# Performance work log

Hardware: AMD Instinct MI355X
Metric: run time of the kernel (lower is better)

Reference implementation:

```python
import jax, jax.numpy as jnp
import numpy as np


def _ln(x, g, b):
    m = x.mean(-1, keepdims=True)
    v = x.var(-1, keepdims=True)
    return (x - m) * jax.lax.rsqrt(v + 1e-5) * g + b


def _shift(x):
    # RWKV time-shift: xx[t] = x[t-1], xx[0] = 0
    return jnp.pad(x, ((0, 0), (1, 0), (0, 0)))[:, :-1]


def setup_inputs() -> dict:
    key = jax.random.key(0)
    ks = jax.random.split(key, 20)
    B, S, D, E, F = 2, 2048, 1024, 8, 2048
    s = 0.02
    return dict(
        x=jax.random.normal(ks[0], (B, S, D), jnp.float32),
        ln1_g=jnp.ones((D,), jnp.float32), ln1_b=jnp.zeros((D,), jnp.float32),
        ln2_g=jnp.ones((D,), jnp.float32), ln2_b=jnp.zeros((D,), jnp.float32),
        tm_mu_k=jax.random.uniform(ks[1], (D,), jnp.float32),
        tm_mu_v=jax.random.uniform(ks[2], (D,), jnp.float32),
        tm_mu_r=jax.random.uniform(ks[3], (D,), jnp.float32),
        time_decay=jax.random.normal(ks[4], (D,), jnp.float32) * 0.1,
        time_first=jax.random.normal(ks[5], (D,), jnp.float32) * 0.1,
        Wk=jax.random.normal(ks[6], (D, D), jnp.float32) * s,
        Wv=jax.random.normal(ks[7], (D, D), jnp.float32) * s,
        Wr=jax.random.normal(ks[8], (D, D), jnp.float32) * s,
        Wo=jax.random.normal(ks[9], (D, D), jnp.float32) * s,
        router_w=jax.random.normal(ks[10], (D, E), jnp.float32) * s,
        cm_mu_k=jax.random.uniform(ks[11], (E, D), jnp.float32),
        cm_mu_r=jax.random.uniform(ks[12], (E, D), jnp.float32),
        eWk=jax.random.normal(ks[13], (E, D, F), jnp.float32) * s,
        eWv=jax.random.normal(ks[14], (E, F, D), jnp.float32) * s,
        eWr=jax.random.normal(ks[15], (E, D, D), jnp.float32) * s,
    )


def reference(x, ln1_g, ln1_b, ln2_g, ln2_b, tm_mu_k, tm_mu_v, tm_mu_r,
              time_decay, time_first, Wk, Wv, Wr, Wo, router_w,
              cm_mu_k, cm_mu_r, eWk, eWv, eWr):
    TOP_K = 2
    E = router_w.shape[1]
    B, S, D = x.shape

    # ---- TimeMix on ln1(x) ----
    xn = _ln(x, ln1_g, ln1_b)
    xx = _shift(xn)
    xk = xn * tm_mu_k + xx * (1.0 - tm_mu_k)
    xv = xn * tm_mu_v + xx * (1.0 - tm_mu_v)
    xr = xn * tm_mu_r + xx * (1.0 - tm_mu_r)
    k = xk @ Wk  # [B,S,D]
    v = xv @ Wv
    r = jax.nn.sigmoid(xr @ Wr)

    w = -jnp.exp(time_decay)  # per-channel decay < 0
    u = time_first

    def step(carry, kv_t):
        aa, bb, pp = carry
        kt, vt = kv_t
        qq = jnp.maximum(pp, u + kt)
        e1 = jnp.exp(pp - qq)
        e2 = jnp.exp(u + kt - qq)
        wkv_t = (e1 * aa + e2 * vt) / (e1 * bb + e2)
        qq2 = jnp.maximum(pp + w, kt)
        e1b = jnp.exp(pp + w - qq2)
        e2b = jnp.exp(kt - qq2)
        return (e1b * aa + e2b * vt, e1b * bb + e2b, qq2), wkv_t

    init = (jnp.zeros((B, D), x.dtype), jnp.zeros((B, D), x.dtype),
            jnp.full((B, D), -1e30, x.dtype))
    _, wkv = jax.lax.scan(step, init,
                          (k.transpose(1, 0, 2), v.transpose(1, 0, 2)))
    wkv = wkv.transpose(1, 0, 2)  # [B,S,D]
    x = x + (r * wkv) @ Wo  # residual

    # ---- Router on ln2(x) ----
    ei = _ln(x, ln2_g, ln2_b)
    probs = jax.nn.softmax(ei @ router_w, axis=-1)  # [B,S,E]
    vals, idx = jax.lax.top_k(probs, TOP_K)
    wts = vals / vals.sum(-1, keepdims=True)
    # dense per-token per-expert combine weight [B,S,E]
    tw = jnp.sum(jax.nn.one_hot(idx, E, dtype=x.dtype) * wts[..., None], axis=-2)

    # ---- Dense per-expert ChannelMix (every expert over full tensor) ----
    exx = _shift(ei)
    mk = cm_mu_k[:, None, None, :]  # [E,1,1,D]
    mr = cm_mu_r[:, None, None, :]
    xk_e = ei[None] * mk + exx[None] * (1.0 - mk)  # [E,B,S,D]
    xr_e = ei[None] * mr + exx[None] * (1.0 - mr)
    k_e = jnp.square(jax.nn.relu(jnp.einsum('ebsd,edf->ebsf', xk_e, eWk)))
    kv_e = jnp.einsum('ebsf,efd->ebsd', k_e, eWv)
    r_e = jax.nn.sigmoid(jnp.einsum('ebsd,edg->ebsg', xr_e, eWr))
    expert_out = r_e * kv_e  # [E,B,S,D]
    moe = jnp.einsum('ebsd,bse->bsd', expert_out, tw)
    return x + moe
```

## Files before the change

### kernel.cpp

```cpp
#include <hip/hip_runtime.h>
#include <hip/hip_bf16.h>
#include <stdint.h>

#define DEVI __device__ __forceinline__

typedef __attribute__((ext_vector_type(4))) float f32x4;
typedef __attribute__((ext_vector_type(8))) short short8;
typedef __attribute__((ext_vector_type(4))) short s16x4;

constexpr int B_ = 2, S_ = 2048, D_ = 1024, E_ = 8, F_ = 2048;
constexpr int M_ = B_ * S_;
constexpr int PC_ = 10240;
constexpr int NC_ = 64, L_ = 32;
constexpr int HB_ = 16;
constexpr size_t MD_ = (size_t)M_ * D_;
constexpr size_t DD_ = (size_t)D_ * D_;

DEVI short f2bf(float f) {
  uint32_t u = __float_as_uint(f);
  u = (u + 0x7fffu + ((u >> 16) & 1u)) >> 16;
  return (short)u;
}
DEVI float bf2f(short s) { return __uint_as_float(((uint32_t)(uint16_t)s) << 16); }
struct BfPair { short hi, lo; };
DEVI BfPair split2(float f) {
  BfPair p;
  p.hi = f2bf(f);
  p.lo = f2bf(f - bf2f(p.hi));
  return p;
}

DEVI void gload_lds16(const void* g, void* l) {
  __builtin_amdgcn_global_load_lds(
      (const __attribute__((address_space(1))) unsigned int*)g,
      (__attribute__((address_space(3))) unsigned int*)l, 16, 0, 0);
}

#define MFMA(a, b, c) __builtin_amdgcn_mfma_f32_16x16x32_bf16((a), (b), (c), 0, 0, 0)

__global__ __launch_bounds__(256) void lnmix_kernel(
    const float* __restrict__ x, const float* __restrict__ g,
    const float* __restrict__ b, const float* __restrict__ muk,
    const float* __restrict__ muv, const float* __restrict__ mur,
    short* __restrict__ xk, short* __restrict__ xv, short* __restrict__ xr) {
  int row = blockIdx.x;
  int tx = threadIdx.x;
  int s = row & (S_ - 1);
  size_t o = (size_t)row * D_ + tx * 4;
  f32x4 cur = *(const f32x4*)(x + o);
  f32x4 prv = {0.f, 0.f, 0.f, 0.f};
  if (s > 0) prv = *(const f32x4*)(x + o - D_);
  float a0 = cur[0] + cur[1] + cur[2] + cur[3];
  float a1 = cur[0] * cur[0] + cur[1] * cur[1] + cur[2] * cur[2] + cur[3] * cur[3];
  float a2 = prv[0] + prv[1] + prv[2] + prv[3];
  float a3 = prv[0] * prv[0] + prv[1] * prv[1] + prv[2] * prv[2] + prv[3] * prv[3];
#pragma unroll
  for (int o2 = 32; o2; o2 >>= 1) {
    a0 += __shfl_down(a0, o2);
    a1 += __shfl_down(a1, o2);
    a2 += __shfl_down(a2, o2);
    a3 += __shfl_down(a3, o2);
  }
  __shared__ float rd[4][4];
  if ((tx & 63) == 0) {
    rd[tx >> 6][0] = a0; rd[tx >> 6][1] = a1;
    rd[tx >> 6][2] = a2; rd[tx >> 6][3] = a3;
  }
  __syncthreads();
  a0 = rd[0][0] + rd[1][0] + rd[2][0] + rd[3][0];
  a1 = rd[0][1] + rd[1][1] + rd[2][1] + rd[3][1];
  a2 = rd[0][2] + rd[1][2] + rd[2][2] + rd[3][2];
  a3 = rd[0][3] + rd[1][3] + rd[2][3] + rd[3][3];
  float mc = a0 * (1.0f / D_);
  float rc = rsqrtf(a1 * (1.0f / D_) - mc * mc + 1e-5f);
  float mp = a2 * (1.0f / D_);
  float rp = rsqrtf(a3 * (1.0f / D_) - mp * mp + 1e-5f);
  int d = tx * 4;
  f32x4 gg = *(const f32x4*)(g + d);
  f32x4 bb = *(const f32x4*)(b + d);
  f32x4 mk = *(const f32x4*)(muk + d);
  f32x4 mv = *(const f32x4*)(muv + d);
  f32x4 mr = *(const f32x4*)(mur + d);
  s16x4 okh, okl, ovh, ovl, orh, orl;
#pragma unroll
  for (int j = 0; j < 4; j++) {
    float c = (cur[j] - mc) * rc * gg[j] + bb[j];
    float p = (s > 0) ? (prv[j] - mp) * rp * gg[j] + bb[j] : 0.f;
    BfPair pk = split2(c * mk[j] + p * (1.f - mk[j]));
    BfPair pv = split2(c * mv[j] + p * (1.f - mv[j]));
    BfPair pr = split2(c * mr[j] + p * (1.f - mr[j]));
    okh[j] = pk.hi; okl[j] = pk.lo;
    ovh[j] = pv.hi; ovl[j] = pv.lo;
    orh[j] = pr.hi; orl[j] = pr.lo;
  }
  *(s16x4*)(xk + o) = okh;
  *(s16x4*)(xk + MD_ + o) = okl;
  *(s16x4*)(xv + o) = ovh;
  *(s16x4*)(xv + MD_ + o) = ovl;
  *(s16x4*)(xr + o) = orh;
  *(s16x4*)(xr + MD_ + o) = orl;
}

__global__ __launch_bounds__(256) void ln2_router(
    const float* __restrict__ x, const float* __restrict__ P,
    const float* __restrict__ g, const float* __restrict__ b,
    const float* __restrict__ rw, float* __restrict__ xout,
    float* __restrict__ ei, int* __restrict__ idx2, float* __restrict__ wts2) {
  int row = blockIdx.x;
  int tx = threadIdx.x;
  size_t o = (size_t)row * D_ + tx * 4;
  f32x4 v = *(const f32x4*)(x + o);
  f32x4 p0 = *(const f32x4*)(P + o);
  f32x4 p1 = *(const f32x4*)(P + MD_ + o);
#pragma unroll
  for (int j = 0; j < 4; j++) v[j] += p0[j] + p1[j];
  *(f32x4*)(xout + o) = v;
  float s = v[0] + v[1] + v[2] + v[3];
  float s2 = v[0] * v[0] + v[1] * v[1] + v[2] * v[2] + v[3] * v[3];
#pragma unroll
  for (int of = 32; of; of >>= 1) {
    s += __shfl_down(s, of);
    s2 += __shfl_down(s2, of);
  }
  __shared__ float w1[4], w2[4];
  if ((tx & 63) == 0) { w1[tx >> 6] = s; w2[tx >> 6] = s2; }
  __syncthreads();
  s = w1[0] + w1[1] + w1[2] + w1[3];
  s2 = w2[0] + w2[1] + w2[2] + w2[3];
  float mean = s * (1.0f / D_);
  float rstd = rsqrtf(s2 * (1.0f / D_) - mean * mean + 1e-5f);
  f32x4 gg = *(const f32x4*)(g + tx * 4);
  f32x4 bb = *(const f32x4*)(b + tx * 4);
  f32x4 oo;
#pragma unroll
  for (int j = 0; j < 4; j++) oo[j] = (v[j] - mean) * rstd * gg[j] + bb[j];
  *(f32x4*)(ei + o) = oo;
  float pl[8] = {};
  const float* rr = rw + (size_t)(tx * 4) * 8;
#pragma unroll
  for (int j = 0; j < 4; j++)
#pragma unroll
    for (int e = 0; e < 8; e++) pl[e] += oo[j] * rr[j * 8 + e];
#pragma unroll
  for (int of = 32; of; of >>= 1)
#pragma unroll
    for (int e = 0; e < 8; e++) pl[e] += __shfl_down(pl[e], of);
  __shared__ float plw[4][8];
  if ((tx & 63) == 0)
#pragma unroll
    for (int e = 0; e < 8; e++) plw[tx >> 6][e] = pl[e];
  __syncthreads();
  if (tx == 0) {
    float p8[8];
#pragma unroll
    for (int e = 0; e < 8; e++)
      p8[e] = plw[0][e] + plw[1][e] + plw[2][e] + plw[3][e];
    float mx = p8[0];
#pragma unroll
    for (int e = 1; e < 8; e++) mx = fmaxf(mx, p8[e]);
    float pr[8];
#pragma unroll
    for (int e = 0; e < 8; e++) pr[e] = __expf(p8[e] - mx);
    int i1 = 0;
#pragma unroll
    for (int e = 1; e < 8; e++)
      if (pr[e] > pr[i1]) i1 = e;
    int i2 = (i1 == 0) ? 1 : 0;
#pragma unroll
    for (int e = 0; e < 8; e++)
      if (e != i1 && pr[e] > pr[i2]) i2 = e;
    float v1 = pr[i1], v2 = pr[i2];
    float inv = 1.f / (v1 + v2);
    int t = row;
    idx2[t * 2] = i1;
    idx2[t * 2 + 1] = i2;
    wts2[t * 2] = v1 * inv;
    wts2[t * 2 + 1] = v2 * inv;
  }
}

__global__ __launch_bounds__(512) void hist_kernel(const int* __restrict__ idx2,
                                                   int* __restrict__ pos2,
                                                   int* __restrict__ blockcnt) {
  __shared__ int cnt[8];
  int tx = threadIdx.x;
  if (tx < 8) cnt[tx] = 0;
  __syncthreads();
  int entry = blockIdx.x * 512 + tx;
  int e = idx2[entry];
  pos2[entry] = atomicAdd(&cnt[e], 1);
  __syncthreads();
  if (tx < 8) blockcnt[blockIdx.x * 8 + tx] = cnt[tx];
}

__global__ __launch_bounds__(128) void scan_kernel(const int* __restrict__ blockcnt,
                                                   int* __restrict__ offs,
                                                   int* __restrict__ counts,
                                                   int* __restrict__ gbase) {
  __shared__ int c[HB_][8];
  __shared__ int tot[8];
  __shared__ int eoff[9];
  int tx = threadIdx.x;
  c[tx >> 3][tx & 7] = blockcnt[tx];
  __syncthreads();
  if (tx < 8) {
    int s = 0;
    for (int b2 = 0; b2 < HB_; b2++) {
      int v = c[b2][tx];
      c[b2][tx] = s;
      s += v;
    }
    tot[tx] = s;
    counts[tx] = s;
  }
  __syncthreads();
  if (tx == 0) {
    int o = 0;
    for (int e = 0; e < 8; e++) {
      eoff[e] = o;
      o += ((tot[e] + 255) >> 8) << 8;
    }
    eoff[8] = o;
    for (int e = 0; e < 9; e++) offs[e] = eoff[e];
  }
  __syncthreads();
  gbase[tx] = eoff[tx & 7] + c[tx >> 3][tx & 7];
}

__global__ __launch_bounds__(256) void slot_kernel(const int* __restrict__ idx2,
                                                   const int* __restrict__ pos2,
                                                   const int* __restrict__ gbase,
                                                   int* __restrict__ elist,
                                                   int* __restrict__ slots) {
  int entry = blockIdx.x * 256 + threadIdx.x;
  int e = idx2[entry];
  int slot = gbase[(entry >> 9) * 8 + e] + pos2[entry];
  elist[slot] = entry >> 1;
  slots[entry] = slot;
}

template <int SPLIT>
__global__ __launch_bounds__(256) void transpose_cvt(const float* __restrict__ in,
                                                     short* __restrict__ out, int R,
                                                     int C) {
  __shared__ float t[32][33];
  size_t PS = (size_t)R * C;
  const float* inm = in + (size_t)blockIdx.z * PS;
  short* outm = out + (size_t)blockIdx.z * PS * (SPLIT ? 2 : 1);
  int r = threadIdx.x >> 3;
  int c4 = (threadIdx.x & 7) * 4;
  f32x4 v = *(const f32x4*)(inm + (size_t)(blockIdx.y * 32 + r) * C + blockIdx.x * 32 + c4);
#pragma unroll
  for (int i = 0; i < 4; i++) t[r][c4 + i] = v[i];
  __syncthreads();
  s16x4 oh, ol;
#pragma unroll
  for (int i = 0; i < 4; i++) {
    float val = t[c4 + i][r];
    if (SPLIT) {
      BfPair p = split2(val);
      oh[i] = p.hi;
      ol[i] = p.lo;
    } else {
      oh[i] = f2bf(val);
    }
  }
  size_t oidx = (size_t)(blockIdx.x * 32 + r) * R + blockIdx.y * 32 + c4;
  *(s16x4*)(outm + oidx) = oh;
  if (SPLIT) *(s16x4*)(outm + PS + oidx) = ol;
}

__global__ __launch_bounds__(256) void transpose_cvt4(
    const float* __restrict__ w0, const float* __restrict__ w1,
    const float* __restrict__ w2, const float* __restrict__ w3,
    short* __restrict__ out) {
  __shared__ float t[32][33];
  int z = blockIdx.z;
  const float* inm = (z == 0) ? w0 : (z == 1) ? w1 : (z == 2) ? w2 : w3;
  short* outm = out + (size_t)z * (2 * DD_);
  int r = threadIdx.x >> 3;
  int c4 = (threadIdx.x & 7) * 4;
  f32x4 v = *(const f32x4*)(inm + (size_t)(blockIdx.y * 32 + r) * D_ + blockIdx.x * 32 + c4);
#pragma unroll
  for (int i = 0; i < 4; i++) t[r][c4 + i] = v[i];
  __syncthreads();
  s16x4 oh, ol;
#pragma unroll
  for (int i = 0; i < 4; i++) {
    BfPair p = split2(t[c4 + i][r]);
    oh[i] = p.hi;
    ol[i] = p.lo;
  }
  size_t oidx = (size_t)(blockIdx.x * 32 + r) * D_ + blockIdx.y * 32 + c4;
  *(s16x4*)(outm + oidx) = oh;
  *(s16x4*)(outm + DD_ + oidx) = ol;
}


__global__ __launch_bounds__(512) void gemm_kvr(const short* __restrict__ X,
                                                const short* __restrict__ W,
                                                float* __restrict__ KVR) {
  __shared__ __align__(16) short Ah[256 * 32], Al[256 * 32];
  __shared__ __align__(16) short Bh[128 * 32], Bl[128 * 32];
  int tx = threadIdx.x;
  int lane = tx & 63;
  int orig = blockIdx.x + (blockIdx.y << 3) + (blockIdx.z << 7);
  int wgid = (orig & 7) * 48 + (orig >> 3);
  int z = wgid >> 7;
  int rem = wgid & 127;
  int colStart = (rem & 7) * 128;
  int rowStart = (rem >> 3) * 256;
  const short* A0 = X + (size_t)z * (2 * MD_) + (size_t)rowStart * D_;
  const short* B0 = W + (size_t)z * (2 * DD_) + (size_t)colStart * D_;
  float* C = KVR + (size_t)z * MD_;
  int wave = tx >> 6, wm = wave >> 1, wn = wave & 1;
  f32x4 acc[4][4] = {};
  for (int k0 = 0; k0 < D_; k0 += 32) {
#pragma unroll
    for (int i = 0; i < 2; i++) {
      int c = i * 512 + tx;
      int row = c >> 2;
      int kb = (c & 3) * 16;
      size_t go = (size_t)row * (D_ * 2) + (size_t)k0 * 2 + kb;
      size_t lo = (size_t)(i * 512 + (tx & ~63)) * 16;
      gload_lds16((const char*)A0 + go, (char*)Ah + lo);
      gload_lds16((const char*)A0 + MD_ * 2 + go, (char*)Al + lo);
    }
    {
      int row = tx >> 2;
      int kb = (tx & 3) * 16;
      size_t go = (size_t)row * (D_ * 2) + (size_t)k0 * 2 + kb;
      size_t lo = (size_t)(tx & ~63) * 16;
      gload_lds16((const char*)B0 + go, (char*)Bh + lo);
      gload_lds16((const char*)B0 + DD_ * 2 + go, (char*)Bl + lo);
    }
    __syncthreads();
    short8 a[4], a2[4], b[4], b2[4];
#pragma unroll
    for (int m = 0; m < 4; m++) {
      int ro = (wm * 64 + m * 16 + (lane & 15)) * 32 + (lane >> 4) * 8;
      a[m] = *(const short8*)(Ah + ro);
      a2[m] = *(const short8*)(Al + ro);
    }
#pragma unroll
    for (int n = 0; n < 4; n++) {
      int ro = (wn * 64 + n * 16 + (lane & 15)) * 32 + (lane >> 4) * 8;
      b[n] = *(const short8*)(Bh + ro);
      b2[n] = *(const short8*)(Bl + ro);
    }
#pragma unroll
    for (int m = 0; m < 4; m++)
#pragma unroll
      for (int n = 0; n < 4; n++) {
        acc[m][n] = MFMA(a[m], b[n], acc[m][n]);
        acc[m][n] = MFMA(a2[m], b[n], acc[m][n]);
        acc[m][n] = MFMA(a[m], b2[n], acc[m][n]);
      }
    __syncthreads();
  }
  int r0 = rowStart + wm * 64 + ((lane >> 4) << 2);
  int cgl = colStart + wn * 64 + (lane & 15);
#pragma unroll
  for (int m = 0; m < 4; m++)
#pragma unroll
    for (int n = 0; n < 4; n++)
#pragma unroll
      for (int j = 0; j < 4; j++) {
        size_t idx = (size_t)(r0 + m * 16 + j) * D_ + cgl + n * 16;
        float vv = acc[m][n][j];
        if (z == 2) vv = 1.0f / (1.0f + __expf(-vv));
        C[idx] = vv;
      }
}

__global__ __launch_bounds__(512) void gemm_wo(const short* __restrict__ A,
                                               const short* __restrict__ Bt,
                                               float* __restrict__ P) {
  __shared__ __align__(16) short Ah[256 * 32], Al[256 * 32];
  __shared__ __align__(16) short Bh[128 * 32], Bl[128 * 32];
  int tx = threadIdx.x;
  int lane = tx & 63;
  int orig = blockIdx.x + (blockIdx.y << 3) + (blockIdx.z << 7);
  int wgid = (orig & 7) * 32 + (orig >> 3);
  int z = wgid >> 7;
  int rem = wgid & 127;
  int colStart = (rem & 7) * 128;
  int rowStart = (rem >> 3) * 256;
  const short* A0 = A + (size_t)rowStart * D_;
  const short* B0 = Bt + (size_t)colStart * D_;
  float* C = P + (size_t)z * MD_;
  int wave = tx >> 6, wm = wave >> 1, wn = wave & 1;
  f32x4 acc[4][4] = {};
  int kbase = z * (D_ / 2);
  for (int k0 = kbase; k0 < kbase + D_ / 2; k0 += 32) {
#pragma unroll
    for (int i = 0; i < 2; i++) {
      int c = i * 512 + tx;
      int row = c >> 2;
      int kb = (c & 3) * 16;
      size_t go = (size_t)row * (D_ * 2) + (size_t)k0 * 2 + kb;
      size_t lo = (size_t)(i * 512 + (tx & ~63)) * 16;
      gload_lds16((const char*)A0 + go, (char*)Ah + lo);
      gload_lds16((const char*)A0 + MD_ * 2 + go, (char*)Al + lo);
    }
    {
      int row = tx >> 2;
      int kb = (tx & 3) * 16;
      size_t go = (size_t)row * (D_ * 2) + (size_t)k0 * 2 + kb;
      size_t lo = (size_t)(tx & ~63) * 16;
      gload_lds16((const char*)B0 + go, (char*)Bh + lo);
      gload_lds16((const char*)B0 + DD_ * 2 + go, (char*)Bl + lo);
    }
    __syncthreads();
    short8 a[4], a2[4], b[4], b2[4];
#pragma unroll
    for (int m = 0; m < 4; m++) {
      int ro = (wm * 64 + m * 16 + (lane & 15)) * 32 + (lane >> 4) * 8;
      a[m] = *(const short8*)(Ah + ro);
      a2[m] = *(const short8*)(Al + ro);
    }
#pragma unroll
    for (int n = 0; n < 4; n++) {
      int ro = (wn * 64 + n * 16 + (lane & 15)) * 32 + (lane >> 4) * 8;
      b[n] = *(const short8*)(Bh + ro);
      b2[n] = *(const short8*)(Bl + ro);
    }
#pragma unroll
    for (int m = 0; m < 4; m++)
#pragma unroll
      for (int n = 0; n < 4; n++) {
        acc[m][n] = MFMA(a[m], b[n], acc[m][n]);
        acc[m][n] = MFMA(a2[m], b[n], acc[m][n]);
        acc[m][n] = MFMA(a[m], b2[n], acc[m][n]);
      }
    __syncthreads();
  }
  int r0 = rowStart + wm * 64 + ((lane >> 4) << 2);
  int cgl = colStart + wn * 64 + (lane & 15);
#pragma unroll
  for (int m = 0; m < 4; m++)
#pragma unroll
    for (int n = 0; n < 4; n++)
#pragma unroll
      for (int j = 0; j < 4; j++)
        C[(size_t)(r0 + m * 16 + j) * D_ + cgl + n * 16] = acc[m][n][j];
}

__global__ __launch_bounds__(512) void gemm_exA(const short* __restrict__ A,
                                                const short* __restrict__ Bt,
                                                short* __restrict__ C,
                                                const int* __restrict__ offs) {
  __shared__ __align__(16) short As[256 * 32];
  __shared__ __align__(16) short Bs[128 * 32];
  int tx = threadIdx.x;
  int lane = tx & 63;
  int orig = blockIdx.x + (blockIdx.y << 4);
  int wgid = (orig & 7) * 80 + (orig >> 3);
  int colStart = (wgid & 15) * 128;
  int rowStart = (wgid >> 4) * 256;
  if (rowStart >= offs[8]) return;
  int e = 0;
  while (e < 7 && rowStart >= offs[e + 1]) e++;
  const short* Ag = A + (size_t)rowStart * D_;
  const short* Bg = Bt + (size_t)e * F_ * D_ + (size_t)colStart * D_;
  int wave = tx >> 6, wm = wave >> 1, wn = wave & 1;
  f32x4 acc[4][4] = {};
  for (int k0 = 0; k0 < D_; k0 += 32) {
#pragma unroll
    for (int i = 0; i < 2; i++) {
      int c = i * 512 + tx;
      int row = c >> 2;
      int kb = (c & 3) * 16;
      size_t go = (size_t)row * (D_ * 2) + (size_t)k0 * 2 + kb;
      size_t lo = (size_t)(i * 512 + (tx & ~63)) * 16;
      gload_lds16((const char*)Ag + go, (char*)As + lo);
    }
    {
      int row = tx >> 2;
      int kb = (tx & 3) * 16;
      size_t go = (size_t)row * (D_ * 2) + (size_t)k0 * 2 + kb;
      size_t lo = (size_t)(tx & ~63) * 16;
      gload_lds16((const char*)Bg + go, (char*)Bs + lo);
    }
    __syncthreads();
    short8 a[4], b[4];
#pragma unroll
    for (int m = 0; m < 4; m++)
      a[m] = *(const short8*)(As + (wm * 64 + m * 16 + (lane & 15)) * 32 + (lane >> 4) * 8);
#pragma unroll
    for (int n = 0; n < 4; n++)
      b[n] = *(const short8*)(Bs + (wn * 64 + n * 16 + (lane & 15)) * 32 + (lane >> 4) * 8);
#pragma unroll
    for (int m = 0; m < 4; m++)
#pragma unroll
      for (int n = 0; n < 4; n++)
        acc[m][n] = MFMA(a[m], b[n], acc[m][n]);
    __syncthreads();
  }
  int r0 = rowStart + wm * 64 + ((lane >> 4) << 2);
  int cgl = colStart + wn * 64 + (lane & 15);
#pragma unroll
  for (int m = 0; m < 4; m++)
#pragma unroll
    for (int n = 0; n < 4; n++)
#pragma unroll
      for (int j = 0; j < 4; j++) {
        size_t idx = (size_t)(r0 + m * 16 + j) * F_ + cgl + n * 16;
        float vv = acc[m][n][j];
        vv = vv > 0.f ? vv * vv : 0.f;
        C[idx] = f2bf(vv);
      }
}

__global__ __launch_bounds__(512) void gemm_ex2(
    const short* __restrict__ h, const short* __restrict__ eWvT,
    short* __restrict__ kvb, const short* __restrict__ Ar,
    const short* __restrict__ eWrT, short* __restrict__ rrb,
    const int* __restrict__ offs) {
  __shared__ __align__(16) short As[256 * 32];
  __shared__ __align__(16) short Bs[128 * 32];
  int tx = threadIdx.x;
  int lane = tx & 63;
  int zz = blockIdx.z;
  int orig = blockIdx.x + (blockIdx.y << 3);
  int wgid = (orig & 7) * 40 + (orig >> 3);
  int colStart = (wgid & 7) * 128;
  int rowStart = (wgid >> 3) * 256;
  if (rowStart >= offs[8]) return;
  int e = 0;
  while (e < 7 && rowStart >= offs[e + 1]) e++;
  int K = zz ? D_ : F_;
  const short* Ag = (zz ? Ar : h) + (size_t)rowStart * K;
  const short* Bg = (zz ? eWrT : eWvT) + (size_t)e * D_ * K + (size_t)colStart * K;
  short* C = zz ? rrb : kvb;
  int wave = tx >> 6, wm = wave >> 1, wn = wave & 1;
  f32x4 acc[4][4] = {};
  for (int k0 = 0; k0 < K; k0 += 32) {
#pragma unroll
    for (int i = 0; i < 2; i++) {
      int c = i * 512 + tx;
      int row = c >> 2;
      int kb = (c & 3) * 16;
      size_t go = (size_t)row * ((size_t)K * 2) + (size_t)k0 * 2 + kb;
      size_t lo = (size_t)(i * 512 + (tx & ~63)) * 16;
      gload_lds16((const char*)Ag + go, (char*)As + lo);
    }
    {
      int row = tx >> 2;
      int kb = (tx & 3) * 16;
      size_t go = (size_t)row * ((size_t)K * 2) + (size_t)k0 * 2 + kb;
      size_t lo = (size_t)(tx & ~63) * 16;
      gload_lds16((const char*)Bg + go, (char*)Bs + lo);
    }
    __syncthreads();
    short8 a[4], b[4];
#pragma unroll
    for (int m = 0; m < 4; m++)
      a[m] = *(const short8*)(As + (wm * 64 + m * 16 + (lane & 15)) * 32 + (lane >> 4) * 8);
#pragma unroll
    for (int n = 0; n < 4; n++)
      b[n] = *(const short8*)(Bs + (wn * 64 + n * 16 + (lane & 15)) * 32 + (lane >> 4) * 8);
#pragma unroll
    for (int m = 0; m < 4; m++)
#pragma unroll
      for (int n = 0; n < 4; n++)
        acc[m][n] = MFMA(a[m], b[n], acc[m][n]);
    __syncthreads();
  }
  int r0 = rowStart + wm * 64 + ((lane >> 4) << 2);
  int cgl = colStart + wn * 64 + (lane & 15);
#pragma unroll
  for (int m = 0; m < 4; m++)
#pragma unroll
    for (int n = 0; n < 4; n++)
#pragma unroll
      for (int j = 0; j < 4; j++) {
        size_t idx = (size_t)(r0 + m * 16 + j) * D_ + cgl + n * 16;
        float vv = acc[m][n][j];
        if (zz) vv = 1.0f / (1.0f + __expf(-vv));
        C[idx] = f2bf(vv);
      }
}

__global__ __launch_bounds__(256) void wkv_chunk_kernel(const float* __restrict__ k,
                                                        const float* __restrict__ v,
                                                        const float* __restrict__ td,
                                                        float* __restrict__ chA,
                                                        float* __restrict__ chB) {
  int d = blockIdx.x * 256 + threadIdx.x;
  int c = blockIdx.y;
  int b = blockIdx.z;
  float w = -__expf(td[d]);
  float dec = __expf(w);
  float A = 0.f, Bb = 0.f;
  size_t base = ((size_t)b * S_ + (size_t)c * L_) * D_ + d;
  for (int i = 0; i < L_; i++) {
    float kt = k[base + (size_t)i * D_];
    float vt = v[base + (size_t)i * D_];
    float ek = __expf(kt);
    A = fmaf(A, dec, ek * vt);
    Bb = fmaf(Bb, dec, ek);
  }
  size_t o = ((size_t)b * NC_ + c) * D_ + d;
  chA[o] = A;
  chB[o] = Bb;
}

__global__ __launch_bounds__(256) void wkv_carry_kernel(const float* __restrict__ chA,
                                                        const float* __restrict__ chB,
                                                        const float* __restrict__ td,
                                                        float* __restrict__ caA,
                                                        float* __restrict__ caB) {
  int d = blockIdx.x * 256 + threadIdx.x;
  int b = blockIdx.y;
  float w = -__expf(td[d]);
  float decL = __expf(w * (float)L_);
  float A = 0.f, Bb = 0.f;
  for (int c = 0; c < NC_; c++) {
    size_t o = ((size_t)b * NC_ + c) * D_ + d;
    caA[o] = A;
    caB[o] = Bb;
    A = fmaf(A, decL, chA[o]);
    Bb = fmaf(Bb, decL, chB[o]);
  }
}

__global__ __launch_bounds__(256) void wkv_out_kernel(
    const float* __restrict__ k, const float* __restrict__ v,
    const float* __restrict__ r, const float* __restrict__ caA,
    const float* __restrict__ caB, const float* __restrict__ td,
    const float* __restrict__ tf, short* __restrict__ rwkv) {
  int d = blockIdx.x * 256 + threadIdx.x;
  int c = blockIdx.y;
  int b = blockIdx.z;
  float w = -__expf(td[d]);
  float dec = __expf(w);
  float eu = __expf(tf[d]);
  size_t co = ((size_t)b * NC_ + c) * D_ + d;
  float A = caA[co], Bb = caB[co];
  size_t base = ((size_t)b * S_ + (size_t)c * L_) * D_ + d;
  for (int i = 0; i < L_; i++) {
    size_t ix = base + (size_t)i * D_;
    float kt = k[ix], vt = v[ix], rt = r[ix];
    float ek = __expf(kt);
    float euk = eu * ek;
    float wkv = (A + euk * vt) / (Bb + euk);
    BfPair p = split2(rt * wkv);
    rwkv[ix] = p.hi;
    rwkv[MD_ + ix] = p.lo;
    A = fmaf(A, dec, ek * vt);
    Bb = fmaf(Bb, dec, ek);
  }
}

__global__ __launch_bounds__(256) void gather_mix_kernel(
    const float* __restrict__ ei, const float* __restrict__ cmk,
    const float* __restrict__ cmr, const int* __restrict__ offs,
    const int* __restrict__ counts, const int* __restrict__ elist,
    short* __restrict__ Ak, short* __restrict__ Ar) {
  int row = blockIdx.x;
  if (row >= offs[8]) return;
  int e = 0;
  while (e < 7 && row >= offs[e + 1]) e++;
  int p = row - offs[e];
  int d = threadIdx.x * 4;
  size_t ro = (size_t)row * D_ + d;
  if (p >= counts[e]) {
    s16x4 z = {0, 0, 0, 0};
    *(s16x4*)(Ak + ro) = z;
    *(s16x4*)(Ar + ro) = z;
    return;
  }
  int t = elist[row];
  int s = t & (S_ - 1);
  f32x4 cur = *(const f32x4*)(ei + (size_t)t * D_ + d);
  f32x4 prev = {0.f, 0.f, 0.f, 0.f};
  if (s > 0) prev = *(const f32x4*)(ei + (size_t)(t - 1) * D_ + d);
  f32x4 mk = *(const f32x4*)(cmk + (size_t)e * D_ + d);
  f32x4 mr = *(const f32x4*)(cmr + (size_t)e * D_ + d);
  s16x4 ok, orr;
#pragma unroll
  for (int j = 0; j < 4; j++) {
    ok[j] = f2bf(cur[j] * mk[j] + prev[j] * (1.f - mk[j]));
    orr[j] = f2bf(cur[j] * mr[j] + prev[j] * (1.f - mr[j]));
  }
  *(s16x4*)(Ak + ro) = ok;
  *(s16x4*)(Ar + ro) = orr;
}

__global__ __launch_bounds__(256) void final_kernel(
    const float* __restrict__ xout, const short* __restrict__ rrb,
    const short* __restrict__ kvb, const int* __restrict__ slots,
    const float* __restrict__ wts2, float* __restrict__ out) {
  size_t i4 = (size_t)blockIdx.x * 256 + threadIdx.x;
  size_t el = i4 * 4;
  int t = (int)(el >> 10);
  int d = (int)(el & (D_ - 1));
  int s0 = slots[t * 2], s1 = slots[t * 2 + 1];
  float w0 = wts2[t * 2], w1 = wts2[t * 2 + 1];
  f32x4 xo = *(const f32x4*)(xout + el);
  s16x4 r0 = *(const s16x4*)(rrb + (size_t)s0 * D_ + d);
  s16x4 k0 = *(const s16x4*)(kvb + (size_t)s0 * D_ + d);
  s16x4 r1 = *(const s16x4*)(rrb + (size_t)s1 * D_ + d);
  s16x4 k1 = *(const s16x4*)(kvb + (size_t)s1 * D_ + d);
  f32x4 o;
#pragma unroll
  for (int j = 0; j < 4; j++)
    o[j] = xo[j] + w0 * bf2f(r0[j]) * bf2f(k0[j]) + w1 * bf2f(r1[j]) * bf2f(k1[j]);
  *(f32x4*)(out + el) = o;
}

extern "C" void kernel_launch(void* const* d_in, const int* in_sizes, int n_in,
                              void* d_out, int out_size, void* d_ws, size_t ws_size,
                              hipStream_t stream) {
  (void)in_sizes; (void)n_in; (void)out_size; (void)ws_size;
  const float* x = (const float*)d_in[0];
  const float* ln1g = (const float*)d_in[1];
  const float* ln1b = (const float*)d_in[2];
  const float* ln2g = (const float*)d_in[3];
  const float* ln2b = (const float*)d_in[4];
  const float* muk = (const float*)d_in[5];
  const float* muv = (const float*)d_in[6];
  const float* mur = (const float*)d_in[7];
  const float* tdec = (const float*)d_in[8];
  const float* tfirst = (const float*)d_in[9];
  const float* Wk = (const float*)d_in[10];
  const float* Wv = (const float*)d_in[11];
  const float* Wr = (const float*)d_in[12];
  const float* Wo = (const float*)d_in[13];
  const float* rw = (const float*)d_in[14];
  const float* cmk = (const float*)d_in[15];
  const float* cmr = (const float*)d_in[16];
  const float* eWk = (const float*)d_in[17];
  const float* eWv = (const float*)d_in[18];
  const float* eWr = (const float*)d_in[19];
  float* out = (float*)d_out;

  char* w = (char*)d_ws;
  size_t off = 0;
  auto alloc = [&](size_t bytes) {
    size_t o = off;
    off = (off + bytes + 255) & ~(size_t)255;
    return o;
  };
  const size_t szDD2x2 = DD_ * 2 * 2;
  size_t o_WT = alloc(4 * szDD2x2);
  size_t o_WkT = o_WT, o_WoT = o_WT + 3 * szDD2x2;
  size_t o_eWkT = alloc((size_t)E_ * D_ * F_ * 2);
  size_t o_eWvT = alloc((size_t)E_ * F_ * D_ * 2);
  size_t o_eWrT = alloc((size_t)E_ * D_ * D_ * 2);
  size_t o_xout = alloc(MD_ * 4);
  size_t o_ei = alloc(MD_ * 4);
  size_t o_counts = alloc(64);
  size_t o_offs = alloc(64);
  size_t o_idx2 = alloc((size_t)M_ * 2 * 4);
  size_t o_wts2 = alloc((size_t)M_ * 2 * 4);
  size_t o_pos2 = alloc((size_t)M_ * 2 * 4);
  size_t o_blockcnt = alloc((size_t)HB_ * 8 * 4);
  size_t o_gbase = alloc((size_t)HB_ * 8 * 4);
  size_t o_elist = alloc((size_t)PC_ * 4);
  size_t o_slots = alloc((size_t)M_ * 2 * 4);
  size_t poolBase = off;
  size_t off1 = poolBase;
  auto alloc1 = [&](size_t bytes) {
    size_t o = off1;
    off1 = (off1 + bytes + 255) & ~(size_t)255;
    return o;
  };
  size_t o_rwkv = alloc1(MD_ * 2 * 2);
  size_t o_xk = alloc1(MD_ * 2 * 2);
  size_t o_xv = alloc1(MD_ * 2 * 2);
  size_t o_xr = alloc1(MD_ * 2 * 2);
  size_t o_k = alloc1(MD_ * 4);
  size_t o_v = alloc1(MD_ * 4);
  size_t o_r = alloc1(MD_ * 4);
  size_t o_chA = alloc1((size_t)B_ * NC_ * D_ * 4);
  size_t o_chB = alloc1((size_t)B_ * NC_ * D_ * 4);
  size_t o_caA = alloc1((size_t)B_ * NC_ * D_ * 4);
  size_t o_caB = alloc1((size_t)B_ * NC_ * D_ * 4);
  size_t o_P = o_k;
  size_t off2 = poolBase;
  auto alloc2 = [&](size_t bytes) {
    size_t o = off2;
    off2 = (off2 + bytes + 255) & ~(size_t)255;
    return o;
  };
  size_t o_Ak = alloc2((size_t)PC_ * D_ * 2);
  size_t o_Ar = alloc2((size_t)PC_ * D_ * 2);
  size_t o_h = alloc2((size_t)PC_ * F_ * 2);
  size_t o_kvb = alloc2((size_t)PC_ * D_ * 2);
  size_t o_rrb = alloc2((size_t)PC_ * D_ * 2);

#define WP(T, o) ((T*)(w + (o)))

  transpose_cvt4<<<dim3(32, 32, 4), 256, 0, stream>>>(Wk, Wv, Wr, Wo,
                                                      WP(short, o_WkT));
  transpose_cvt<0><<<dim3(F_ / 32, D_ / 32, E_), 256, 0, stream>>>(eWk, WP(short, o_eWkT), D_, F_);
  transpose_cvt<0><<<dim3(D_ / 32, F_ / 32, E_), 256, 0, stream>>>(eWv, WP(short, o_eWvT), F_, D_);
  transpose_cvt<0><<<dim3(D_ / 32, D_ / 32, E_), 256, 0, stream>>>(eWr, WP(short, o_eWrT), D_, D_);

  lnmix_kernel<<<M_, 256, 0, stream>>>(x, ln1g, ln1b, muk, muv, mur,
                                       WP(short, o_xk), WP(short, o_xv),
                                       WP(short, o_xr));

  gemm_kvr<<<dim3(8, 16, 3), 512, 0, stream>>>(WP(short, o_xk), WP(short, o_WkT),
                                               WP(float, o_k));

  wkv_chunk_kernel<<<dim3(D_ / 256, NC_, B_), 256, 0, stream>>>(
      WP(float, o_k), WP(float, o_v), tdec, WP(float, o_chA), WP(float, o_chB));
  wkv_carry_kernel<<<dim3(D_ / 256, B_), 256, 0, stream>>>(
      WP(float, o_chA), WP(float, o_chB), tdec, WP(float, o_caA), WP(float, o_caB));
  wkv_out_kernel<<<dim3(D_ / 256, NC_, B_), 256, 0, stream>>>(
      WP(float, o_k), WP(float, o_v), WP(float, o_r), WP(float, o_caA),
      WP(float, o_caB), tdec, tfirst, WP(short, o_rwkv));

  gemm_wo<<<dim3(8, 16, 2), 512, 0, stream>>>(WP(short, o_rwkv), WP(short, o_WoT),
                                              WP(float, o_P));
  ln2_router<<<M_, 256, 0, stream>>>(x, WP(float, o_P), ln2g, ln2b, rw,
                                     WP(float, o_xout), WP(float, o_ei),
                                     WP(int, o_idx2), WP(float, o_wts2));

  hist_kernel<<<HB_, 512, 0, stream>>>(WP(int, o_idx2), WP(int, o_pos2),
                                       WP(int, o_blockcnt));
  scan_kernel<<<1, 128, 0, stream>>>(WP(int, o_blockcnt), WP(int, o_offs),
                                     WP(int, o_counts), WP(int, o_gbase));
  slot_kernel<<<(2 * M_) / 256, 256, 0, stream>>>(WP(int, o_idx2), WP(int, o_pos2),
                                                  WP(int, o_gbase), WP(int, o_elist),
                                                  WP(int, o_slots));
  gather_mix_kernel<<<PC_, 256, 0, stream>>>(WP(float, o_ei), cmk, cmr, WP(int, o_offs),
                                             WP(int, o_counts), WP(int, o_elist),
                                             WP(short, o_Ak), WP(short, o_Ar));

  gemm_exA<<<dim3(16, 40), 512, 0, stream>>>(WP(short, o_Ak), WP(short, o_eWkT),
                                             WP(short, o_h), WP(int, o_offs));
  gemm_ex2<<<dim3(8, 40, 2), 512, 0, stream>>>(
      WP(short, o_h), WP(short, o_eWvT), WP(short, o_kvb), WP(short, o_Ar),
      WP(short, o_eWrT), WP(short, o_rrb), WP(int, o_offs));

  final_kernel<<<M_ * D_ / 4 / 256, 256, 0, stream>>>(
      WP(float, o_xout), WP(short, o_rrb), WP(short, o_kvb), WP(int, o_slots),
      WP(float, o_wts2), out);
#undef WP
}
```

Before: 442.5 us.

## Double-buffer LDS tiles in GEMMs and serialize split-bf16 terms as stages

All four MFMA GEMM kernels now use two LDS buffers and prefetch the next K-slice while computing the current one, with one barrier per step instead of two. The hi/lo split-bf16 GEMMs no longer load four tiles and issue three MFMAs per step. Instead they iterate over the three (hi·hi, lo·hi, hi·lo) products as separate stages of a longer single-MFMA loop. The goal is to hide global-load latency behind compute, at the cost of doubled LDS use per block, which may reduce occupancy.

```diff
diff --git a/kernel.cpp b/kernel.cpp
--- a/kernel.cpp
+++ b/kernel.cpp
@@ -300,8 +300,8 @@
 __global__ __launch_bounds__(512) void gemm_kvr(const short* __restrict__ X,
                                                 const short* __restrict__ W,
                                                 float* __restrict__ KVR) {
-  __shared__ __align__(16) short Ah[256 * 32], Al[256 * 32];
-  __shared__ __align__(16) short Bh[128 * 32], Bl[128 * 32];
+  __shared__ __align__(16) short As[2][256 * 32];
+  __shared__ __align__(16) short Bs[2][128 * 32];
   int tx = threadIdx.x;
   int lane = tx & 63;
   int orig = blockIdx.x + (blockIdx.y << 3) + (blockIdx.z << 7);
@@ -310,53 +310,44 @@
   int rem = wgid & 127;
   int colStart = (rem & 7) * 128;
   int rowStart = (rem >> 3) * 256;
-  const short* A0 = X + (size_t)z * (2 * MD_) + (size_t)rowStart * D_;
-  const short* B0 = W + (size_t)z * (2 * DD_) + (size_t)colStart * D_;
+  const char* A0 = (const char*)(X + (size_t)z * (2 * MD_) + (size_t)rowStart * D_);
+  const char* B0 = (const char*)(W + (size_t)z * (2 * DD_) + (size_t)colStart * D_);
   float* C = KVR + (size_t)z * MD_;
   int wave = tx >> 6, wm = wave >> 1, wn = wave & 1;
-  f32x4 acc[4][4] = {};
-  for (int k0 = 0; k0 < D_; k0 += 32) {
+  constexpr int PAm[3] = {0, 1, 0}, PBm[3] = {0, 0, 1};
+  auto stage = [&](int buf, int s) {
+    int term = s >> 5;
+    size_t kb2 = (size_t)((s & 31) << 6);
+    const char* Ap = A0 + (size_t)PAm[term] * (MD_ * 2);
+    const char* Bp = B0 + (size_t)PBm[term] * (DD_ * 2);
 #pragma unroll
     for (int i = 0; i < 2; i++) {
       int c = i * 512 + tx;
-      int row = c >> 2;
-      int kb = (c & 3) * 16;
-      size_t go = (size_t)row * (D_ * 2) + (size_t)k0 * 2 + kb;
-      size_t lo = (size_t)(i * 512 + (tx & ~63)) * 16;
-      gload_lds16((const char*)A0 + go, (char*)Ah + lo);
-      gload_lds16((const char*)A0 + MD_ * 2 + go, (char*)Al + lo);
+      gload_lds16(Ap + (size_t)(c >> 2) * (D_ * 2) + kb2 + (c & 3) * 16,
+                  (char*)As[buf] + (size_t)(i * 512 + (tx & ~63)) * 16);
     }
-    {
-      int row = tx >> 2;
-      int kb = (tx & 3) * 16;
-      size_t go = (size_t)row * (D_ * 2) + (size_t)k0 * 2 + kb;
-      size_t lo = (size_t)(tx & ~63) * 16;
-      gload_lds16((const char*)B0 + go, (char*)Bh + lo);
-      gload_lds16((const char*)B0 + DD_ * 2 + go, (char*)Bl + lo);
-    }
+    gload_lds16(Bp + (size_t)(tx >> 2) * (D_ * 2) + kb2 + (tx & 3) * 16,
+                (char*)Bs[buf] + (size_t)(tx & ~63) * 16);
+  };
+  f32x4 acc[4][4] = {};
+  int cur = 0;
+  stage(0, 0);
+  __syncthreads();
+  for (int s = 0; s < 96; s++) {
+    if (s + 1 < 96) stage(cur ^ 1, s + 1);
+    short8 a[4], b[4];
+#pragma unroll
+    for (int m = 0; m < 4; m++)
+      a[m] = *(const short8*)(As[cur] + (wm * 64 + m * 16 + (lane & 15)) * 32 + (lane >> 4) * 8);
+#pragma unroll
+    for (int n = 0; n < 4; n++)
+      b[n] = *(const short8*)(Bs[cur] + (wn * 64 + n * 16 + (lane & 15)) * 32 + (lane >> 4) * 8);
+#pragma unroll
+    for (int m = 0; m < 4; m++)
+#pragma unroll
+      for (int n = 0; n < 4; n++) acc[m][n] = MFMA(a[m], b[n], acc[m][n]);
     __syncthreads();
-    short8 a[4], a2[4], b[4], b2[4];
-#pragma unroll
-    for (int m = 0; m < 4; m++) {
-      int ro = (wm * 64 + m * 16 + (lane & 15)) * 32 + (lane >> 4) * 8;
-      a[m] = *(const short8*)(Ah + ro);
-      a2[m] = *(const short8*)(Al + ro);
-    }
-#pragma unroll
-    for (int n = 0; n < 4; n++) {
-      int ro = (wn * 64 + n * 16 + (lane & 15)) * 32 + (lane >> 4) * 8;
-      b[n] = *(const short8*)(Bh + ro);
-      b2[n] = *(const short8*)(Bl + ro);
-    }
-#pragma unroll
-    for (int m = 0; m < 4; m++)
-#pragma unroll
-      for (int n = 0; n < 4; n++) {
-        acc[m][n] = MFMA(a[m], b[n], acc[m][n]);
-        acc[m][n] = MFMA(a2[m], b[n], acc[m][n]);
-        acc[m][n] = MFMA(a[m], b2[n], acc[m][n]);
-      }
-    __syncthreads();
+    cur ^= 1;
   }
   int r0 = rowStart + wm * 64 + ((lane >> 4) << 2);
   int cgl = colStart + wn * 64 + (lane & 15);
@@ -376,8 +367,8 @@
 __global__ __launch_bounds__(512) void gemm_wo(const short* __restrict__ A,
                                                const short* __restrict__ Bt,
                                                float* __restrict__ P) {
-  __shared__ __align__(16) short Ah[256 * 32], Al[256 * 32];
-  __shared__ __align__(16) short Bh[128 * 32], Bl[128 * 32];
+  __shared__ __align__(16) short As[2][256 * 32];
+  __shared__ __align__(16) short Bs[2][128 * 32];
   int tx = threadIdx.x;
   int lane = tx & 63;
   int orig = blockIdx.x + (blockIdx.y << 3) + (blockIdx.z << 7);
@@ -386,54 +377,45 @@
   int rem = wgid & 127;
   int colStart = (rem & 7) * 128;
   int rowStart = (rem >> 3) * 256;
-  const short* A0 = A + (size_t)rowStart * D_;
-  const short* B0 = Bt + (size_t)colStart * D_;
+  const char* A0 = (const char*)(A + (size_t)rowStart * D_);
+  const char* B0 = (const char*)(Bt + (size_t)colStart * D_);
   float* C = P + (size_t)z * MD_;
   int wave = tx >> 6, wm = wave >> 1, wn = wave & 1;
-  f32x4 acc[4][4] = {};
-  int kbase = z * (D_ / 2);
-  for (int k0 = kbase; k0 < kbase + D_ / 2; k0 += 32) {
+  size_t kbase = (size_t)z * (D_);
+  constexpr int PAm[3] = {0, 1, 0}, PBm[3] = {0, 0, 1};
+  auto stage = [&](int buf, int s) {
+    int term = s >> 4;
+    size_t kb2 = kbase + (size_t)((s & 15) << 6);
+    const char* Ap = A0 + (size_t)PAm[term] * (MD_ * 2);
+    const char* Bp = B0 + (size_t)PBm[term] * (DD_ * 2);
 #pragma unroll
     for (int i = 0; i < 2; i++) {
       int c = i * 512 + tx;
-      int row = c >> 2;
-      int kb = (c & 3) * 16;
-      size_t go = (size_t)row * (D_ * 2) + (size_t)k0 * 2 + kb;
-      size_t lo = (size_t)(i * 512 + (tx & ~63)) * 16;
-      gload_lds16((const char*)A0 + go, (char*)Ah + lo);
-      gload_lds16((const char*)A0 + MD_ * 2 + go, (char*)Al + lo);
+      gload_lds16(Ap + (size_t)(c >> 2) * (D_ * 2) + kb2 + (c & 3) * 16,
+                  (char*)As[buf] + (size_t)(i * 512 + (tx & ~63)) * 16);
     }
-    {
-      int row = tx >> 2;
-      int kb = (tx & 3) * 16;
-      size_t go = (size_t)row * (D_ * 2) + (size_t)k0 * 2 + kb;
-      size_t lo = (size_t)(tx & ~63) * 16;
-      gload_lds16((const char*)B0 + go, (char*)Bh + lo);
-      gload_lds16((const char*)B0 + DD_ * 2 + go, (char*)Bl + lo);
-    }
+    gload_lds16(Bp + (size_t)(tx >> 2) * (D_ * 2) + kb2 + (tx & 3) * 16,
+                (char*)Bs[buf] + (size_t)(tx & ~63) * 16);
+  };
+  f32x4 acc[4][4] = {};
+  int cur = 0;
+  stage(0, 0);
+  __syncthreads();
+  for (int s = 0; s < 48; s++) {
+    if (s + 1 < 48) stage(cur ^ 1, s + 1);
+    short8 a[4], b[4];
+#pragma unroll
+    for (int m = 0; m < 4; m++)
+      a[m] = *(const short8*)(As[cur] + (wm * 64 + m * 16 + (lane & 15)) * 32 + (lane >> 4) * 8);
+#pragma unroll
+    for (int n = 0; n < 4; n++)
+      b[n] = *(const short8*)(Bs[cur] + (wn * 64 + n * 16 + (lane & 15)) * 32 + (lane >> 4) * 8);
+#pragma unroll
+    for (int m = 0; m < 4; m++)
+#pragma unroll
+      for (int n = 0; n < 4; n++) acc[m][n] = MFMA(a[m], b[n], acc[m][n]);
     __syncthreads();
-    short8 a[4], a2[4], b[4], b2[4];
-#pragma unroll
-    for (int m = 0; m < 4; m++) {
-      int ro = (wm * 64 + m * 16 + (lane & 15)) * 32 + (lane >> 4) * 8;
-      a[m] = *(const short8*)(Ah + ro);
-      a2[m] = *(const short8*)(Al + ro);
-    }
-#pragma unroll
-    for (int n = 0; n < 4; n++) {
-      int ro = (wn * 64 + n * 16 + (lane & 15)) * 32 + (lane >> 4) * 8;
-      b[n] = *(const short8*)(Bh + ro);
-      b2[n] = *(const short8*)(Bl + ro);
-    }
-#pragma unroll
-    for (int m = 0; m < 4; m++)
-#pragma unroll
-      for (int n = 0; n < 4; n++) {
-        acc[m][n] = MFMA(a[m], b[n], acc[m][n]);
-        acc[m][n] = MFMA(a2[m], b[n], acc[m][n]);
-        acc[m][n] = MFMA(a[m], b2[n], acc[m][n]);
-      }
-    __syncthreads();
+    cur ^= 1;
   }
   int r0 = rowStart + wm * 64 + ((lane >> 4) << 2);
   int cgl = colStart + wn * 64 + (lane & 15);
@@ -450,8 +432,8 @@
                                                 const short* __restrict__ Bt,
                                                 short* __restrict__ C,
                                                 const int* __restrict__ offs) {
-  __shared__ __align__(16) short As[256 * 32];
-  __shared__ __align__(16) short Bs[128 * 32];
+  __shared__ __align__(16) short As[2][256 * 32];
+  __shared__ __align__(16) short Bs[2][128 * 32];
   int tx = threadIdx.x;
   int lane = tx & 63;
   int orig = blockIdx.x + (blockIdx.y << 4);
@@ -461,41 +443,39 @@
   if (rowStart >= offs[8]) return;
   int e = 0;
   while (e < 7 && rowStart >= offs[e + 1]) e++;
-  const short* Ag = A + (size_t)rowStart * D_;
-  const short* Bg = Bt + (size_t)e * F_ * D_ + (size_t)colStart * D_;
+  const char* Ag = (const char*)(A + (size_t)rowStart * D_);
+  const char* Bg = (const char*)(Bt + (size_t)e * F_ * D_ + (size_t)colStart * D_);
   int wave = tx >> 6, wm = wave >> 1, wn = wave & 1;
-  f32x4 acc[4][4] = {};
-  for (int k0 = 0; k0 < D_; k0 += 32) {
+  auto stage = [&](int buf, int s) {
+    size_t kb2 = (size_t)s << 6;
 #pragma unroll
     for (int i = 0; i < 2; i++) {
       int c = i * 512 + tx;
-      int row = c >> 2;
-      int kb = (c & 3) * 16;
-      size_t go = (size_t)row * (D_ * 2) + (size_t)k0 * 2 + kb;
-      size_t lo = (size_t)(i * 512 + (tx & ~63)) * 16;
-      gload_lds16((const char*)Ag + go, (char*)As + lo);
+      gload_lds16(Ag + (size_t)(c >> 2) * (D_ * 2) + kb2 + (c & 3) * 16,
+                  (char*)As[buf] + (size_t)(i * 512 + (tx & ~63)) * 16);
     }
-    {
-      int row = tx >> 2;
-      int kb = (tx & 3) * 16;
-      size_t go = (size_t)row * (D_ * 2) + (size_t)k0 * 2 + kb;
-      size_t lo = (size_t)(tx & ~63) * 16;
-      gload_lds16((const char*)Bg + go, (char*)Bs + lo);
-    }
+    gload_lds16(Bg + (size_t)(tx >> 2) * (D_ * 2) + kb2 + (tx & 3) * 16,
+                (char*)Bs[buf] + (size_t)(tx & ~63) * 16);
+  };
+  f32x4 acc[4][4] = {};
+  int cur = 0;
+  stage(0, 0);
+  __syncthreads();
+  for (int s = 0; s < 32; s++) {
+    if (s + 1 < 32) stage(cur ^ 1, s + 1);
+    short8 a[4], b[4];
+#pragma unroll
+    for (int m = 0; m < 4; m++)
+      a[m] = *(const short8*)(As[cur] + (wm * 64 + m * 16 + (lane & 15)) * 32 + (lane >> 4) * 8);
+#pragma unroll
+    for (int n = 0; n < 4; n++)
+      b[n] = *(const short8*)(Bs[cur] + (wn * 64 + n * 16 + (lane & 15)) * 32 + (lane >> 4) * 8);
+#pragma unroll
+    for (int m = 0; m < 4; m++)
+#pragma unroll
+      for (int n = 0; n < 4; n++) acc[m][n] = MFMA(a[m], b[n], acc[m][n]);
     __syncthreads();
-    short8 a[4], b[4];
-#pragma unroll
-    for (int m = 0; m < 4; m++)
-      a[m] = *(const short8*)(As + (wm * 64 + m * 16 + (lane & 15)) * 32 + (lane >> 4) * 8);
-#pragma unroll
-    for (int n = 0; n < 4; n++)
-      b[n] = *(const short8*)(Bs + (wn * 64 + n * 16 + (lane & 15)) * 32 + (lane >> 4) * 8);
-#pragma unroll
-    for (int m = 0; m < 4; m++)
-#pragma unroll
-      for (int n = 0; n < 4; n++)
-        acc[m][n] = MFMA(a[m], b[n], acc[m][n]);
-    __syncthreads();
+    cur ^= 1;
   }
   int r0 = rowStart + wm * 64 + ((lane >> 4) << 2);
   int cgl = colStart + wn * 64 + (lane & 15);
@@ -517,8 +497,8 @@
     short* __restrict__ kvb, const short* __restrict__ Ar,
     const short* __restrict__ eWrT, short* __restrict__ rrb,
     const int* __restrict__ offs) {
-  __shared__ __align__(16) short As[256 * 32];
-  __shared__ __align__(16) short Bs[128 * 32];
+  __shared__ __align__(16) short As[2][256 * 32];
+  __shared__ __align__(16) short Bs[2][128 * 32];
   int tx = threadIdx.x;
   int lane = tx & 63;
   int zz = blockIdx.z;
@@ -530,43 +510,43 @@
   int e = 0;
   while (e < 7 && rowStart >= offs[e + 1]) e++;
   int K = zz ? D_ : F_;
-  const short* Ag = (zz ? Ar : h) + (size_t)rowStart * K;
-  const short* Bg = (zz ? eWrT : eWvT) + (size_t)e * D_ * K + (size_t)colStart * K;
-  short* C = zz ? rrb : kvb;
+  const char* Ag = (const char*)((zz ? Ar : h) + (size_t)rowStart * K);
+  const char* Bg =
+      (const char*)((zz ? eWrT : eWvT) + (size_t)e * D_ * K + (size_t)colStart * K);
   int wave = tx >> 6, wm = wave >> 1, wn = wave & 1;
-  f32x4 acc[4][4] = {};
-  for (int k0 = 0; k0 < K; k0 += 32) {
+  int NS = K / 32;
+  auto stage = [&](int buf, int s) {
+    size_t kb2 = (size_t)s << 6;
 #pragma unroll
     for (int i = 0; i < 2; i++) {
       int c = i * 512 + tx;
-      int row = c >> 2;
-      int kb = (c & 3) * 16;
-      size_t go = (size_t)row * ((size_t)K * 2) + (size_t)k0 * 2 + kb;
-      size_t lo = (size_t)(i * 512 + (tx & ~63)) * 16;
-      gload_lds16((const char*)Ag + go, (char*)As + lo);
+      gload_lds16(Ag + (size_t)(c >> 2) * ((size_t)K * 2) + kb2 + (c & 3) * 16,
+                  (char*)As[buf] + (size_t)(i * 512 + (tx & ~63)) * 16);
     }
-    {
-      int row = tx >> 2;
-      int kb = (tx & 3) * 16;
-      size_t go = (size_t)row * ((size_t)K * 2) + (size_t)k0 * 2 + kb;
-      size_t lo = (size_t)(tx & ~63) * 16;
-      gload_lds16((const char*)Bg + go, (char*)Bs + lo);
-    }
+    gload_lds16(Bg + (size_t)(tx >> 2) * ((size_t)K * 2) + kb2 + (tx & 3) * 16,
+                (char*)Bs[buf] + (size_t)(tx & ~63) * 16);
+  };
+  f32x4 acc[4][4] = {};
+  int cur = 0;
+  stage(0, 0);
+  __syncthreads();
+  for (int s = 0; s < NS; s++) {
+    if (s + 1 < NS) stage(cur ^ 1, s + 1);
+    short8 a[4], b[4];
+#pragma unroll
+    for (int m = 0; m < 4; m++)
+      a[m] = *(const short8*)(As[cur] + (wm * 64 + m * 16 + (lane & 15)) * 32 + (lane >> 4) * 8);
+#pragma unroll
+    for (int n = 0; n < 4; n++)
+      b[n] = *(const short8*)(Bs[cur] + (wn * 64 + n * 16 + (lane & 15)) * 32 + (lane >> 4) * 8);
+#pragma unroll
+    for (int m = 0; m < 4; m++)
+#pragma unroll
+      for (int n = 0; n < 4; n++) acc[m][n] = MFMA(a[m], b[n], acc[m][n]);
     __syncthreads();
-    short8 a[4], b[4];
-#pragma unroll
-    for (int m = 0; m < 4; m++)
-      a[m] = *(const short8*)(As + (wm * 64 + m * 16 + (lane & 15)) * 32 + (lane >> 4) * 8);
-#pragma unroll
-    for (int n = 0; n < 4; n++)
-      b[n] = *(const short8*)(Bs + (wn * 64 + n * 16 + (lane & 15)) * 32 + (lane >> 4) * 8);
-#pragma unroll
-    for (int m = 0; m < 4; m++)
-#pragma unroll
-      for (int n = 0; n < 4; n++)
-        acc[m][n] = MFMA(a[m], b[n], acc[m][n]);
-    __syncthreads();
-  }
+    cur ^= 1;
+  }
+  short* C = zz ? rrb : kvb;
   int r0 = rowStart + wm * 64 + ((lane >> 4) << 2);
   int cgl = colStart + wn * 64 + (lane & 15);
 #pragma unroll
```

Result: slower. 464.9 us (+5.1%).
